# Kernel tuning notes

Hardware: AMD Instinct MI355X
Metric: run time of the kernel (lower is better)

## Reference

```python
import jax, jax.numpy as jnp
import numpy as np

JUMP = 0.05      # stride 'jumps'
FILTER = 0.15    # filter_dim per axis
PTS = 20         # arange(0, 1, 0.05) -> 20 positions per dim -> 400 centers


def _centers():
    g = jnp.arange(PTS, dtype=jnp.float32) * JUMP  # start=0, domain=1, direction=+1
    xx, yy = jnp.meshgrid(g, g, indexing="ij")
    return jnp.stack([xx.ravel(), yy.ravel()], axis=-1)  # [400, 2]


def setup_inputs() -> dict:
    key = jax.random.key(0)
    ks = jax.random.split(key, 10)
    B, H, N = 64, 256, 2048
    F = 2    # input_numb_field * output_numb_field = 2*1 kernel nets
    KH = 20  # default kernel hidden width

    def w(k, shape, fan_in):
        return jax.random.normal(k, shape, jnp.float32) / np.sqrt(fan_in)

    return dict(
        weights=jax.random.normal(ks[0], (B, H), jnp.float32),
        grid=jax.random.uniform(ks[1], (N, 2), jnp.float32),
        # FeedForward: H -> 120 -> 240 -> 400, Tanh activations
        ff_w1=w(ks[2], (H, 120), H), ff_b1=jnp.zeros((120,), jnp.float32),
        ff_w2=w(ks[3], (120, 240), 120), ff_b2=jnp.zeros((240,), jnp.float32),
        ff_w3=w(ks[4], (240, 400), 240), ff_b3=jnp.zeros((400,), jnp.float32),
        # per-field kernel MLPs: 2 -> 20 -> 20 -> 1 (ReLU), stacked on F
        k_w1=w(ks[5], (F, 2, KH), 2), k_b1=jnp.zeros((F, KH), jnp.float32),
        k_w2=w(ks[6], (F, KH, KH), KH), k_b2=jnp.zeros((F, KH), jnp.float32),
        k_w3=w(ks[7], (F, KH, 1), KH), k_b3=jnp.zeros((F, 1), jnp.float32),
    )


def reference(weights, grid, ff_w1, ff_b1, ff_w2, ff_b2, ff_w3, ff_b3,
              k_w1, k_b1, k_w2, k_b2, k_w3, k_b3):
    # 1) FeedForward: latent weights -> 400 per-stride integrals
    h = jnp.tanh(weights @ ff_w1 + ff_b1)
    h = jnp.tanh(h @ ff_w2 + ff_b2)
    integ = h @ ff_w3 + ff_b3                       # [B, 400]

    # 2) continuous transpose convolution onto the point cloud `grid`
    centers = _centers()                            # [K=400, 2]
    local = grid[:, None, :] - centers[None, :, :]  # [N, K, 2] filter-local coords
    inside = jnp.all((local >= 0.0) & (local <= FILTER), axis=-1)  # [N, K]

    # kernel MLPs evaluated densely over (point, center) pairs, masked to window
    t = jax.nn.relu(jnp.einsum('nkd,fdh->fnkh', local, k_w1) + k_b1[:, None, None, :])
    t = jax.nn.relu(jnp.einsum('fnkh,fhg->fnkg', t, k_w2) + k_b2[:, None, None, :])
    kval = jnp.einsum('fnkg,fg->fnk', t, k_w3[:, :, 0]) + k_b3[:, :, None]  # [F, N, K]
    kval = jnp.where(inside[None], kval, 0.0)

    # spread integrals through the (masked) continuous filters
    fields = jnp.einsum('fnk,bk->bnf', kval, integ)  # [B, N, F]
    return jax.nn.sigmoid(fields)
```

## Files before the change

kernel.cpp:

```cpp
#include <hip/hip_runtime.h>
#include <math.h>

#define NPTS 2048
#define KDIM 400

__global__ __launch_bounds__(512) void k_ff_and_kval(
    const float* __restrict__ weights, const float* __restrict__ grid,
    const float* __restrict__ ff_w1, const float* __restrict__ ff_b1,
    const float* __restrict__ ff_w2, const float* __restrict__ ff_b2,
    const float* __restrict__ ff_w3, const float* __restrict__ ff_b3,
    const float* __restrict__ k_w1, const float* __restrict__ k_b1,
    const float* __restrict__ k_w2, const float* __restrict__ k_b2,
    const float* __restrict__ k_w3, const float* __restrict__ k_b3,
    float* __restrict__ integ, float* __restrict__ kv0,
    float* __restrict__ kv1, int* __restrict__ kidx)
{
    const int t = threadIdx.x;
    if (blockIdx.x < 128) {
        const int b = blockIdx.x >> 1, half = blockIdx.x & 1;
        __shared__ float wrow[256], h1[120], h2[240];
        __shared__ float p1[4][120], p2[2][240], p3[2][200];

        if (t < 256) wrow[t] = weights[b * 256 + t];
        __syncthreads();

        if (t < 480) {
            const int seg = t / 120, o = t - seg * 120;
            float s = (seg == 0) ? ff_b1[o] : 0.f;
            const int i0 = seg * 64;
            #pragma unroll 16
            for (int i = 0; i < 64; ++i)
                s = fmaf(wrow[i0 + i], ff_w1[(i0 + i) * 120 + o], s);
            p1[seg][o] = s;
        }
        __syncthreads();
        if (t < 120) h1[t] = tanhf(p1[0][t] + p1[1][t] + p1[2][t] + p1[3][t]);
        __syncthreads();

        if (t < 480) {
            const int seg = t / 240, o = t - seg * 240;
            float s = (seg == 0) ? ff_b2[o] : 0.f;
            const int i0 = seg * 60;
            #pragma unroll 15
            for (int i = 0; i < 60; ++i)
                s = fmaf(h1[i0 + i], ff_w2[(i0 + i) * 240 + o], s);
            p2[seg][o] = s;
        }
        __syncthreads();
        if (t < 240) h2[t] = tanhf(p2[0][t] + p2[1][t]);
        __syncthreads();

        if (t < 400) {
            const int seg = t / 200, o = t - seg * 200, oc = half * 200 + o;
            float s = (seg == 0) ? ff_b3[oc] : 0.f;
            const int i0 = seg * 120;
            #pragma unroll 15
            for (int i = 0; i < 120; ++i)
                s = fmaf(h2[i0 + i], ff_w3[(i0 + i) * 400 + oc], s);
            p3[seg][o] = s;
        }
        __syncthreads();
        if (t < 200) integ[b * 400 + half * 200 + t] = p3[0][t] + p3[1][t];
    } else {
        __shared__ float sw1[80], sb1[40], sw2[800], sb2[40], sw3[40], sb3[2];
        for (int i = t; i < 80;  i += 512) sw1[i] = k_w1[i];
        for (int i = t; i < 800; i += 512) sw2[i] = k_w2[i];
        if (t < 40) { sb1[t] = k_b1[t]; sb2[t] = k_b2[t]; sw3[t] = k_w3[t]; }
        if (t < 2)  sb3[t] = k_b3[t];
        __syncthreads();

        const int pid  = blockIdx.x - 128;
        const int f    = t >> 8;
        const int idx  = t & 255;
        const int slot = idx >> 4;
        const int pt   = idx & 15;
        const int n    = pid * 16 + pt;
        const float2 g2 = ((const float2*)grid)[n];
        const float x = g2.x, y = g2.y;
        const int ilx = (int)ceilf((x - 0.15f) * 20.0f - 0.01f);
        const int ily = (int)ceilf((y - 0.15f) * 20.0f - 0.01f);
        const int ix = ilx + (slot >> 2);
        const int iy = ily + (slot & 3);

        float kv = 0.f;
        int k = 0;
        if (ix >= 0 && ix < 20 && iy >= 0 && iy < 20) {
            const float gx = __fmul_rn((float)ix, 0.05f);
            const float gy = __fmul_rn((float)iy, 0.05f);
            const float lx = __fsub_rn(x, gx);
            const float ly = __fsub_rn(y, gy);
            if (lx >= 0.f && lx <= 0.15f && ly >= 0.f && ly <= 0.15f) {
                k = ix * 20 + iy;
                float hv[20];
                #pragma unroll
                for (int hh = 0; hh < 20; ++hh)
                    hv[hh] = fmaxf(0.f,
                        fmaf(lx, sw1[f * 40 + hh],
                        fmaf(ly, sw1[f * 40 + 20 + hh], sb1[f * 20 + hh])));
                float o = sb3[f];
                #pragma unroll
                for (int g = 0; g < 20; ++g) {
                    float s = sb2[f * 20 + g];
                    #pragma unroll
                    for (int hh = 0; hh < 20; ++hh)
                        s = fmaf(hv[hh], sw2[f * 400 + hh * 20 + g], s);
                    o = fmaf(fmaxf(0.f, s), sw3[f * 20 + g], o);
                }
                kv = o;
            }
        }
        (f ? kv1 : kv0)[slot * NPTS + n] = kv;
        if (f == 0) kidx[slot * NPTS + n] = k;
    }
}

__global__ __launch_bounds__(512) void k_field(
    const float* __restrict__ integ, const float* __restrict__ kv0,
    const float* __restrict__ kv1, const int* __restrict__ kidx,
    float2* __restrict__ out)
{
    __shared__ float Li[KDIM];
    const int b  = blockIdx.x >> 2;
    const int n  = (blockIdx.x & 3) * 512 + threadIdx.x;
    if (threadIdx.x < KDIM) Li[threadIdx.x] = integ[b * KDIM + threadIdx.x];
    __syncthreads();

    float a0 = 0.f, a1 = 0.f;
    #pragma unroll
    for (int j = 0; j < 16; ++j) {
        const float w = Li[kidx[j * NPTS + n]];
        a0 = fmaf(kv0[j * NPTS + n], w, a0);
        a1 = fmaf(kv1[j * NPTS + n], w, a1);
    }
    out[b * NPTS + n] = make_float2(1.f / (1.f + __expf(-a0)),
                                    1.f / (1.f + __expf(-a1)));
}

extern "C" void kernel_launch(void* const* d_in, const int* in_sizes, int n_in,
                              void* d_out, int out_size, void* d_ws, size_t ws_size,
                              hipStream_t stream) {
    const float* weights = (const float*)d_in[0];
    const float* grid    = (const float*)d_in[1];
    const float* ff_w1   = (const float*)d_in[2];
    const float* ff_b1   = (const float*)d_in[3];
    const float* ff_w2   = (const float*)d_in[4];
    const float* ff_b2   = (const float*)d_in[5];
    const float* ff_w3   = (const float*)d_in[6];
    const float* ff_b3   = (const float*)d_in[7];
    const float* k_w1    = (const float*)d_in[8];
    const float* k_b1    = (const float*)d_in[9];
    const float* k_w2    = (const float*)d_in[10];
    const float* k_b2    = (const float*)d_in[11];
    const float* k_w3    = (const float*)d_in[12];
    const float* k_b3    = (const float*)d_in[13];

    float* integ = (float*)d_ws;
    float* kv0   = integ + 64 * KDIM;
    float* kv1   = kv0 + 16 * NPTS;
    int*   kidx  = (int*)(kv1 + 16 * NPTS);

    k_ff_and_kval<<<256, 512, 0, stream>>>(
        weights, grid, ff_w1, ff_b1, ff_w2, ff_b2, ff_w3, ff_b3,
        k_w1, k_b1, k_w2, k_b2, k_w3, k_b3,
        integ, kv0, kv1, kidx);

    k_field<<<256, 512, 0, stream>>>(
        integ, kv0, kv1, kidx, (float2*)d_out);
}
```

Before: 15.09 us.

## Pack kernel values and indices into float4 cells and split FMA chains

Replaces the three separate planar arrays (kv0, kv1, kidx) with one interleaved float4 array, so the field kernel reads each slot with a single 16-byte load instead of three 4-byte loads. It also breaks the serial FMA accumulation chains in the feed-forward and kernel-MLP loops into four independent accumulators to expose instruction-level parallelism. The field kernel vectorises the integ staging into shared memory and unrolls the slot loop by two with separate accumulators. Costs are a wasted fourth float per cell, partial float4 writes from two different threads, and summation order that differs slightly from the reference.

New measurement: 15.59 us. 1.03x slower.

```diff
diff --git a/kernel.cpp b/kernel.cpp
--- a/kernel.cpp
+++ b/kernel.cpp
@@ -3,6 +3,8 @@
 
 #define NPTS 2048
 #define KDIM 400
+
+typedef float f32x4 __attribute__((ext_vector_type(4)));
 
 __global__ __launch_bounds__(512) void k_ff_and_kval(
     const float* __restrict__ weights, const float* __restrict__ grid,
@@ -12,8 +14,7 @@
     const float* __restrict__ k_w1, const float* __restrict__ k_b1,
     const float* __restrict__ k_w2, const float* __restrict__ k_b2,
     const float* __restrict__ k_w3, const float* __restrict__ k_b3,
-    float* __restrict__ integ, float* __restrict__ kv0,
-    float* __restrict__ kv1, int* __restrict__ kidx)
+    float* __restrict__ integ, float4* __restrict__ kvp)
 {
     const int t = threadIdx.x;
     if (blockIdx.x < 128) {
@@ -26,12 +27,16 @@
 
         if (t < 480) {
             const int seg = t / 120, o = t - seg * 120;
-            float s = (seg == 0) ? ff_b1[o] : 0.f;
             const int i0 = seg * 64;
-            #pragma unroll 16
-            for (int i = 0; i < 64; ++i)
-                s = fmaf(wrow[i0 + i], ff_w1[(i0 + i) * 120 + o], s);
-            p1[seg][o] = s;
+            float s0 = (seg == 0) ? ff_b1[o] : 0.f, s1 = 0.f, s2 = 0.f, s3 = 0.f;
+            #pragma unroll
+            for (int i = 0; i < 64; i += 4) {
+                s0 = fmaf(wrow[i0+i+0], ff_w1[(i0+i+0) * 120 + o], s0);
+                s1 = fmaf(wrow[i0+i+1], ff_w1[(i0+i+1) * 120 + o], s1);
+                s2 = fmaf(wrow[i0+i+2], ff_w1[(i0+i+2) * 120 + o], s2);
+                s3 = fmaf(wrow[i0+i+3], ff_w1[(i0+i+3) * 120 + o], s3);
+            }
+            p1[seg][o] = (s0 + s1) + (s2 + s3);
         }
         __syncthreads();
         if (t < 120) h1[t] = tanhf(p1[0][t] + p1[1][t] + p1[2][t] + p1[3][t]);
@@ -39,12 +44,16 @@
 
         if (t < 480) {
             const int seg = t / 240, o = t - seg * 240;
-            float s = (seg == 0) ? ff_b2[o] : 0.f;
             const int i0 = seg * 60;
-            #pragma unroll 15
-            for (int i = 0; i < 60; ++i)
-                s = fmaf(h1[i0 + i], ff_w2[(i0 + i) * 240 + o], s);
-            p2[seg][o] = s;
+            float s0 = (seg == 0) ? ff_b2[o] : 0.f, s1 = 0.f, s2 = 0.f, s3 = 0.f;
+            #pragma unroll
+            for (int i = 0; i < 60; i += 4) {
+                s0 = fmaf(h1[i0+i+0], ff_w2[(i0+i+0) * 240 + o], s0);
+                s1 = fmaf(h1[i0+i+1], ff_w2[(i0+i+1) * 240 + o], s1);
+                s2 = fmaf(h1[i0+i+2], ff_w2[(i0+i+2) * 240 + o], s2);
+                s3 = fmaf(h1[i0+i+3], ff_w2[(i0+i+3) * 240 + o], s3);
+            }
+            p2[seg][o] = (s0 + s1) + (s2 + s3);
         }
         __syncthreads();
         if (t < 240) h2[t] = tanhf(p2[0][t] + p2[1][t]);
@@ -52,12 +61,16 @@
 
         if (t < 400) {
             const int seg = t / 200, o = t - seg * 200, oc = half * 200 + o;
-            float s = (seg == 0) ? ff_b3[oc] : 0.f;
             const int i0 = seg * 120;
-            #pragma unroll 15
-            for (int i = 0; i < 120; ++i)
-                s = fmaf(h2[i0 + i], ff_w3[(i0 + i) * 400 + oc], s);
-            p3[seg][o] = s;
+            float s0 = (seg == 0) ? ff_b3[oc] : 0.f, s1 = 0.f, s2 = 0.f, s3 = 0.f;
+            #pragma unroll
+            for (int i = 0; i < 120; i += 4) {
+                s0 = fmaf(h2[i0+i+0], ff_w3[(i0+i+0) * 400 + oc], s0);
+                s1 = fmaf(h2[i0+i+1], ff_w3[(i0+i+1) * 400 + oc], s1);
+                s2 = fmaf(h2[i0+i+2], ff_w3[(i0+i+2) * 400 + oc], s2);
+                s3 = fmaf(h2[i0+i+3], ff_w3[(i0+i+3) * 400 + oc], s3);
+            }
+            p3[seg][o] = (s0 + s1) + (s2 + s3);
         }
         __syncthreads();
         if (t < 200) integ[b * 400 + half * 200 + t] = p3[0][t] + p3[1][t];
@@ -100,40 +113,48 @@
                 float o = sb3[f];
                 #pragma unroll
                 for (int g = 0; g < 20; ++g) {
-                    float s = sb2[f * 20 + g];
+                    float s0 = sb2[f * 20 + g], s1 = 0.f, s2 = 0.f, s3 = 0.f;
                     #pragma unroll
-                    for (int hh = 0; hh < 20; ++hh)
-                        s = fmaf(hv[hh], sw2[f * 400 + hh * 20 + g], s);
-                    o = fmaf(fmaxf(0.f, s), sw3[f * 20 + g], o);
+                    for (int hh = 0; hh < 20; hh += 4) {
+                        s0 = fmaf(hv[hh+0], sw2[f * 400 + (hh+0) * 20 + g], s0);
+                        s1 = fmaf(hv[hh+1], sw2[f * 400 + (hh+1) * 20 + g], s1);
+                        s2 = fmaf(hv[hh+2], sw2[f * 400 + (hh+2) * 20 + g], s2);
+                        s3 = fmaf(hv[hh+3], sw2[f * 400 + (hh+3) * 20 + g], s3);
+                    }
+                    o = fmaf(fmaxf(0.f, (s0 + s1) + (s2 + s3)), sw3[f * 20 + g], o);
                 }
                 kv = o;
             }
         }
-        (f ? kv1 : kv0)[slot * NPTS + n] = kv;
-        if (f == 0) kidx[slot * NPTS + n] = k;
+        float4* cell = &kvp[slot * NPTS + n];
+        if (f == 0) { cell->x = kv; cell->z = __int_as_float(k); }
+        else         cell->y = kv;
     }
 }
 
 __global__ __launch_bounds__(512) void k_field(
-    const float* __restrict__ integ, const float* __restrict__ kv0,
-    const float* __restrict__ kv1, const int* __restrict__ kidx,
+    const float* __restrict__ integ, const float4* __restrict__ kvp,
     float2* __restrict__ out)
 {
     __shared__ float Li[KDIM];
-    const int b  = blockIdx.x >> 2;
-    const int n  = (blockIdx.x & 3) * 512 + threadIdx.x;
-    if (threadIdx.x < KDIM) Li[threadIdx.x] = integ[b * KDIM + threadIdx.x];
+    const int b = blockIdx.x >> 2;
+    const int n = (blockIdx.x & 3) * 512 + threadIdx.x;
+    if (threadIdx.x < KDIM / 4)
+        ((f32x4*)Li)[threadIdx.x] = ((const f32x4*)(integ + b * KDIM))[threadIdx.x];
     __syncthreads();
 
-    float a0 = 0.f, a1 = 0.f;
+    float a0 = 0.f, a1 = 0.f, c0 = 0.f, c1 = 0.f;
     #pragma unroll
-    for (int j = 0; j < 16; ++j) {
-        const float w = Li[kidx[j * NPTS + n]];
-        a0 = fmaf(kv0[j * NPTS + n], w, a0);
-        a1 = fmaf(kv1[j * NPTS + n], w, a1);
+    for (int j = 0; j < 16; j += 2) {
+        const float4 cA = kvp[j * NPTS + n];
+        const float4 cB = kvp[(j + 1) * NPTS + n];
+        const float wA = Li[__float_as_int(cA.z)];
+        const float wB = Li[__float_as_int(cB.z)];
+        a0 = fmaf(cA.x, wA, a0); a1 = fmaf(cA.y, wA, a1);
+        c0 = fmaf(cB.x, wB, c0); c1 = fmaf(cB.y, wB, c1);
     }
-    out[b * NPTS + n] = make_float2(1.f / (1.f + __expf(-a0)),
-                                    1.f / (1.f + __expf(-a1)));
+    out[b * NPTS + n] = make_float2(1.f / (1.f + __expf(-(a0 + c0))),
+                                    1.f / (1.f + __expf(-(a1 + c1))));
 }
 
 extern "C" void kernel_launch(void* const* d_in, const int* in_sizes, int n_in,
@@ -154,16 +175,13 @@
     const float* k_w3    = (const float*)d_in[12];
     const float* k_b3    = (const float*)d_in[13];
 
-    float* integ = (float*)d_ws;
-    float* kv0   = integ + 64 * KDIM;
-    float* kv1   = kv0 + 16 * NPTS;
-    int*   kidx  = (int*)(kv1 + 16 * NPTS);
+    float*  integ = (float*)d_ws;
+    float4* kvp   = (float4*)((char*)d_ws + 64 * KDIM * sizeof(float));
 
     k_ff_and_kval<<<256, 512, 0, stream>>>(
         weights, grid, ff_w1, ff_b1, ff_w2, ff_b2, ff_w3, ff_b3,
         k_w1, k_b1, k_w2, k_b2, k_w3, k_b3,
-        integ, kv0, kv1, kidx);
+        integ, kvp);
 
-    k_field<<<256, 512, 0, stream>>>(
-        integ, kv0, kv1, kidx, (float2*)d_out);
+    k_field<<<256, 512, 0, stream>>>(integ, kvp, (float2*)d_out);
 }
```
